# Kernel optimization log

Measured on AMD Instinct MI355X. Metric: run time of the kernel, lower is better.

## Reference

```python
import jax, jax.numpy as jnp
import numpy as np

VOCAB, EMBED, HIDDEN, NCLASS = 50000, 256, 256, 5
B, T = 64, 512


def _lstm_cell(x, h, c, W, U, b):
    # Keras LSTMCell: gate order i, f, g(candidate), o
    z = x @ W + h @ U + b  # [B, 4H]
    i, f, g, o = jnp.split(z, 4, axis=-1)
    i = jax.nn.sigmoid(i)
    f = jax.nn.sigmoid(f)
    g = jnp.tanh(g)
    o = jax.nn.sigmoid(o)
    c_new = f * c + i * g
    h_new = o * jnp.tanh(c_new)
    return h_new, c_new


def _run_stacked(xs, W1, U1, b1, W2, U2, b2):
    # xs: [T, B, E] -> outputs of layer 2: [T, B, H]
    Bb = xs.shape[1]
    H = U1.shape[0]
    zero = jnp.zeros((Bb, H), dtype=xs.dtype)
    init = (zero, zero, zero, zero)

    def step(carry, x_t):
        h1, c1, h2, c2 = carry
        h1, c1 = _lstm_cell(x_t, h1, c1, W1, U1, b1)
        h2, c2 = _lstm_cell(h1, h2, c2, W2, U2, b2)
        return (h1, c1, h2, c2), h2

    _, ys = jax.lax.scan(step, init, xs)
    return ys


def setup_inputs() -> dict:
    key = jax.random.key(0)
    ks = jax.random.split(key, 16)
    s = 0.05

    def mk(k, shape):
        return (jax.random.normal(k, shape, dtype=jnp.float32) * s)

    inp = {
        "tokens": jax.random.randint(ks[0], (B, T), 0, VOCAB, dtype=jnp.int64),
        "embed_table": mk(ks[1], (VOCAB, EMBED)),
        # forward direction, layer 1 and 2
        "fw_W1": mk(ks[2], (EMBED, 4 * HIDDEN)),
        "fw_U1": mk(ks[3], (HIDDEN, 4 * HIDDEN)),
        "fw_b1": jnp.zeros((4 * HIDDEN,), jnp.float32),
        "fw_W2": mk(ks[4], (HIDDEN, 4 * HIDDEN)),
        "fw_U2": mk(ks[5], (HIDDEN, 4 * HIDDEN)),
        "fw_b2": jnp.zeros((4 * HIDDEN,), jnp.float32),
        # backward direction, layer 1 and 2
        "bw_W1": mk(ks[6], (EMBED, 4 * HIDDEN)),
        "bw_U1": mk(ks[7], (HIDDEN, 4 * HIDDEN)),
        "bw_b1": jnp.zeros((4 * HIDDEN,), jnp.float32),
        "bw_W2": mk(ks[8], (HIDDEN, 4 * HIDDEN)),
        "bw_U2": mk(ks[9], (HIDDEN, 4 * HIDDEN)),
        "bw_b2": jnp.zeros((4 * HIDDEN,), jnp.float32),
        # output dense (2H -> 5), softmax
        "dense_W": mk(ks[10], (2 * HIDDEN, NCLASS)),
        "dense_b": jnp.zeros((NCLASS,), jnp.float32),
    }
    return inp


def reference(tokens, embed_table,
              fw_W1, fw_U1, fw_b1, fw_W2, fw_U2, fw_b2,
              bw_W1, bw_U1, bw_b1, bw_W2, bw_U2, bw_b2,
              dense_W, dense_b):
    emb = embed_table[tokens]                    # [B, T, E]
    xs = jnp.swapaxes(emb, 0, 1)                 # [T, B, E]

    ys_fw = _run_stacked(xs, fw_W1, fw_U1, fw_b1, fw_W2, fw_U2, fw_b2)          # [T,B,H]
    ys_bw = _run_stacked(xs[::-1], bw_W1, bw_U1, bw_b1, bw_W2, bw_U2, bw_b2)[::-1]

    feat = jnp.concatenate([ys_fw, ys_bw], axis=-1)   # [T, B, 2H]
    feat = jnp.swapaxes(feat, 0, 1)                   # [B, T, 2H]
    logits = feat @ dense_W + dense_b                 # [B, T, 5]
    return jax.nn.softmax(logits, axis=-1)
```

## Files before the change

### kernel.cpp

```cpp
#include <hip/hip_runtime.h>

typedef __bf16 bf16;
typedef __bf16 bf16x8 __attribute__((ext_vector_type(8)));
typedef float f32x4 __attribute__((ext_vector_type(4)));
typedef unsigned long long u64;

#define T_LEN 512
#define BATCH 64
#define HID 256
#define LDA 520
#define ZLD 68

#define CTRL_BYTES 4096
#define H1_OFF CTRL_BYTES
#define HSLOT_U64 4096
#define HBUF_BYTES (2 * 3 * HSLOT_U64 * 8)
#define H2_OFF (H1_OFF + HBUF_BYTES)
#define LOG_OFF (H2_OFF + HBUF_BYTES)
#define LOG_BYTES (T_LEN * BATCH * 5 * 4)
#define ZERO_BYTES (LOG_OFF + LOG_BYTES)

#define SMEM_A 66560
#define SMEM_Z 17408
#define SMEM_C 4096
#define SMEM_TAIL 576
#define SMEM_BYTES (SMEM_A + SMEM_Z + SMEM_C + SMEM_TAIL)

__device__ inline uint4 cvt8(const float4* s) {
    float4 a = s[0], b = s[1];
    union { uint4 u; bf16 h[8]; } r;
    r.h[0] = (bf16)a.x; r.h[1] = (bf16)a.y; r.h[2] = (bf16)a.z; r.h[3] = (bf16)a.w;
    r.h[4] = (bf16)b.x; r.h[5] = (bf16)b.y; r.h[6] = (bf16)b.z; r.h[7] = (bf16)b.w;
    return r.u;
}

__global__ void __launch_bounds__(256, 1)
lstm_kernel(const int* __restrict__ tokens,
            const float* __restrict__ embed,
            const float* __restrict__ W1f, const float* __restrict__ U1f, const float* __restrict__ b1f,
            const float* __restrict__ W2f, const float* __restrict__ U2f, const float* __restrict__ b2f,
            const float* __restrict__ W1b, const float* __restrict__ U1b, const float* __restrict__ b1b,
            const float* __restrict__ W2b, const float* __restrict__ U2b, const float* __restrict__ b2b,
            const float* __restrict__ dW,
            char* __restrict__ ws)
{
    extern __shared__ char smem[];
    bf16*  Abuf  = (bf16*)smem;
    float* zLds  = (float*)(smem + SMEM_A);
    float* cLds  = (float*)(smem + SMEM_A + SMEM_Z);
    float* bLds  = (float*)(smem + SMEM_A + SMEM_Z + SMEM_C);
    float* dwLds = bLds + 64;

    const int tid = threadIdx.x;
    const int wg  = blockIdx.x;
    const int dir = wg & 1, layer = (wg >> 1) & 1, sub = wg >> 2;

    const float *Wp, *Up, *bp;
    if (dir == 0) { if (layer == 0) { Wp=W1f; Up=U1f; bp=b1f; } else { Wp=W2f; Up=U2f; bp=b2f; } }
    else          { if (layer == 0) { Wp=W1b; Up=U1b; bp=b1b; } else { Wp=W2b; Up=U2b; bp=b2b; } }

    {
        for (int it = 0; it < 32; ++it) {
            int idx = it * 256 + tid;
            int k = idx >> 4, q4 = idx & 15;
            int g = q4 >> 2, u0 = (q4 & 3) * 4;
            const float* src = (k < 256) ? (Wp + (size_t)k * 1024 + g * 256 + sub * 16 + u0)
                                         : (Up + (size_t)(k - 256) * 1024 + g * 256 + sub * 16 + u0);
            float4 v = *(const float4*)src;
            int c0 = g * 16 + u0;
            Abuf[(c0 + 0) * LDA + k] = (bf16)v.x;
            Abuf[(c0 + 1) * LDA + k] = (bf16)v.y;
            Abuf[(c0 + 2) * LDA + k] = (bf16)v.z;
            Abuf[(c0 + 3) * LDA + k] = (bf16)v.w;
        }
        if (tid < 64) {
            int g = tid >> 4, u = tid & 15;
            bLds[tid] = bp[g * 256 + sub * 16 + u];
        }
        if (tid < 80) {
            int u = tid / 5, c = tid % 5;
            dwLds[tid] = dW[(size_t)(dir * 256 + sub * 16 + u) * 5 + c];
        }
        for (int i = tid; i < 1024; i += 256) cLds[i] = 0.f;
    }
    __syncthreads();

    const int wave = tid >> 6, lane = tid & 63, quad = lane >> 4, ln = lane & 15;
    const int mrow0 = (wave >> 1) * 32, ncol0 = (wave & 1) * 32;
    bf16x8 bfrag[2][16];
#pragma unroll
    for (int nt = 0; nt < 2; ++nt)
#pragma unroll
        for (int kt = 0; kt < 16; ++kt)
            bfrag[nt][kt] = *(const bf16x8*)&Abuf[(ncol0 + nt * 16 + ln) * LDA + kt * 32 + quad * 8];
    __syncthreads();

    u64* h1buf = (u64*)(ws + H1_OFF) + (size_t)dir * 3 * HSLOT_U64;
    u64* h2buf = (u64*)(ws + H2_OFF) + (size_t)dir * 3 * HSLOT_U64;
    u64* hOwn  = (layer == 0) ? h1buf : h2buf;
    float* logits   = (float*)(ws + LOG_OFF);
    unsigned* ctrOwn = (unsigned*)ws + (dir * 2 + layer) * 32;
    unsigned* ctrL1  = (unsigned*)ws + (dir * 2 + 0) * 32;
    unsigned* ctrL2  = (unsigned*)ws + (dir * 2 + 1) * 32;

    const int bA = tid >> 2, qA = tid & 3;

    float4 pf[16];
    int tokB = 0;
    if (layer == 0) {
        const int tt0 = dir ? (T_LEN - 1) : 0;
        int tokA = tokens[bA * T_LEN + tt0];
        const float4* src = (const float4*)(embed + (size_t)tokA * HID + qA * 64);
#pragma unroll
        for (int j = 0; j < 16; ++j) pf[j] = src[j];
        const int tt1 = dir ? (T_LEN - 2) : 1;
        tokB = tokens[bA * T_LEN + tt1];
    }

    for (int s = 0; s < T_LEN; ++s) {
        if (tid == 0) {
            unsigned needOwn = (unsigned)s * 16u;
            while (__hip_atomic_load(ctrOwn, __ATOMIC_RELAXED, __HIP_MEMORY_SCOPE_AGENT) < needOwn) {}
            if (layer == 0 && s >= 3) {
                unsigned needT = (unsigned)(s - 2) * 16u;
                while (__hip_atomic_load(ctrL2, __ATOMIC_RELAXED, __HIP_MEMORY_SCOPE_AGENT) < needT) {}
            }
        }
        __syncthreads();

        u64 hreg[16];
        {
            const u64* hsrc = hOwn + (size_t)(s % 3) * HSLOT_U64;
#pragma unroll
            for (int k = 0; k < 16; ++k)
                hreg[k] = __hip_atomic_load(hsrc + k * 256 + tid, __ATOMIC_RELAXED, __HIP_MEMORY_SCOPE_AGENT);
        }
        if (layer == 0) {
            uint4* dstx = (uint4*)&Abuf[bA * LDA + qA * 64];
#pragma unroll
            for (int j = 0; j < 8; ++j) dstx[j] = cvt8(&pf[2 * j]);
        } else {
            if (tid == 0) {
                unsigned needX = (unsigned)(s + 1) * 16u;
                while (__hip_atomic_load(ctrL1, __ATOMIC_RELAXED, __HIP_MEMORY_SCOPE_AGENT) < needX) {}
            }
            __syncthreads();
            u64 xreg[16];
            const u64* xsrc = h1buf + (size_t)((s + 1) % 3) * HSLOT_U64;
#pragma unroll
            for (int k = 0; k < 16; ++k)
                xreg[k] = __hip_atomic_load(xsrc + k * 256 + tid, __ATOMIC_RELAXED, __HIP_MEMORY_SCOPE_AGENT);
#pragma unroll
            for (int k = 0; k < 16; ++k)
                *(u64*)&Abuf[bA * LDA + k * 16 + qA * 4] = xreg[k];
        }
#pragma unroll
        for (int k = 0; k < 16; ++k)
            *(u64*)&Abuf[bA * LDA + 256 + k * 16 + qA * 4] = hreg[k];
        __syncthreads();

        if (layer == 0) {
            const float4* src = (const float4*)(embed + (size_t)tokB * HID + qA * 64);
#pragma unroll
            for (int j = 0; j < 16; ++j) pf[j] = src[j];
            const int sn2 = (s + 2 < T_LEN) ? s + 2 : T_LEN - 1;
            const int tt2 = dir ? (T_LEN - 1 - sn2) : sn2;
            tokB = tokens[bA * T_LEN + tt2];
        }

        f32x4 acc[2][2];
#pragma unroll
        for (int mi = 0; mi < 2; ++mi)
#pragma unroll
            for (int ni = 0; ni < 2; ++ni) acc[mi][ni] = (f32x4)(0.0f);
#pragma unroll
        for (int kt = 0; kt < 16; ++kt) {
            bf16x8 a0 = *(const bf16x8*)&Abuf[(mrow0 + ln) * LDA + kt * 32 + quad * 8];
            bf16x8 a1 = *(const bf16x8*)&Abuf[(mrow0 + 16 + ln) * LDA + kt * 32 + quad * 8];
            acc[0][0] = __builtin_amdgcn_mfma_f32_16x16x32_bf16(a0, bfrag[0][kt], acc[0][0], 0, 0, 0);
            acc[0][1] = __builtin_amdgcn_mfma_f32_16x16x32_bf16(a0, bfrag[1][kt], acc[0][1], 0, 0, 0);
            acc[1][0] = __builtin_amdgcn_mfma_f32_16x16x32_bf16(a1, bfrag[0][kt], acc[1][0], 0, 0, 0);
            acc[1][1] = __builtin_amdgcn_mfma_f32_16x16x32_bf16(a1, bfrag[1][kt], acc[1][1], 0, 0, 0);
        }
#pragma unroll
        for (int mi = 0; mi < 2; ++mi)
#pragma unroll
            for (int ni = 0; ni < 2; ++ni) {
                int row = mrow0 + mi * 16 + quad * 4;
                int col = ncol0 + ni * 16 + ln;
#pragma unroll
                for (int r = 0; r < 4; ++r)
                    zLds[(row + r) * ZLD + col] = acc[mi][ni][r];
            }
        __syncthreads();

        u64* hdst = hOwn + (size_t)((s + 1) % 3) * HSLOT_U64;
        float hv[4];
        {
            const int b = bA, u0 = qA * 4;
#pragma unroll
            for (int e = 0; e < 4; ++e) {
                int u = u0 + e;
                float zi = zLds[b * ZLD + u]      + bLds[u];
                float zf = zLds[b * ZLD + 16 + u] + bLds[16 + u];
                float zg = zLds[b * ZLD + 32 + u] + bLds[32 + u];
                float zo = zLds[b * ZLD + 48 + u] + bLds[48 + u];
                float ig = 1.f / (1.f + __expf(-zi));
                float fg = 1.f / (1.f + __expf(-zf));
                float gg = 1.f - 2.f / (__expf(2.f * zg) + 1.f);
                float og = 1.f / (1.f + __expf(-zo));
                float cn = fg * cLds[b * 16 + u] + ig * gg;
                cLds[b * 16 + u] = cn;
                hv[e] = og * (1.f - 2.f / (__expf(2.f * cn) + 1.f));
            }
            union { u64 w; bf16 h[4]; } pk;
#pragma unroll
            for (int e = 0; e < 4; ++e) pk.h[e] = (bf16)hv[e];
            __hip_atomic_store(hdst + sub * 256 + tid, pk.w,
                               __ATOMIC_RELAXED, __HIP_MEMORY_SCOPE_AGENT);
        }
        float pr[5];
        if (layer == 1) {
#pragma unroll
            for (int c = 0; c < 5; ++c)
                pr[c] = hv[0] * dwLds[(qA * 4 + 0) * 5 + c] + hv[1] * dwLds[(qA * 4 + 1) * 5 + c]
                      + hv[2] * dwLds[(qA * 4 + 2) * 5 + c] + hv[3] * dwLds[(qA * 4 + 3) * 5 + c];
#pragma unroll
            for (int m = 1; m < 4; m <<= 1)
#pragma unroll
                for (int c = 0; c < 5; ++c) pr[c] += __shfl_xor(pr[c], m);
        }

        asm volatile("s_waitcnt vmcnt(0)" ::: "memory");
        __syncthreads();
        if (tid == 0)
            __hip_atomic_fetch_add(ctrOwn, 1u, __ATOMIC_RELAXED, __HIP_MEMORY_SCOPE_AGENT);

        if (layer == 1 && qA == 0) {
            const int tp = dir ? (T_LEN - 1 - s) : s;
            float* lp = &logits[((size_t)tp * BATCH + bA) * 5];
#pragma unroll
            for (int c = 0; c < 5; ++c) atomicAdd(lp + c, pr[c]);
        }
    }
}

__global__ void __launch_bounds__(256)
softmax_kernel(const char* __restrict__ ws, const float* __restrict__ dB, float* __restrict__ out)
{
    const int gid = blockIdx.x * 256 + threadIdx.x;
    const int b = gid & 63, t = gid >> 6;
    const float* lp = (const float*)(ws + LOG_OFF) + ((size_t)t * BATCH + b) * 5;
    float l[5];
#pragma unroll
    for (int c = 0; c < 5; ++c) l[c] = lp[c] + dB[c];
    float m = l[0];
#pragma unroll
    for (int c = 1; c < 5; ++c) m = fmaxf(m, l[c]);
    float e[5], ssum = 0.f;
#pragma unroll
    for (int c = 0; c < 5; ++c) { e[c] = __expf(l[c] - m); ssum += e[c]; }
    float inv = 1.f / ssum;
    float* o = out + ((size_t)b * T_LEN + t) * 5;
#pragma unroll
    for (int c = 0; c < 5; ++c) o[c] = e[c] * inv;
}

extern "C" void kernel_launch(void* const* d_in, const int* in_sizes, int n_in,
                              void* d_out, int out_size, void* d_ws, size_t ws_size,
                              hipStream_t stream)
{
    const int*   tokens = (const int*)d_in[0];
    const float* embed  = (const float*)d_in[1];
    const float* W1f = (const float*)d_in[2],  *U1f = (const float*)d_in[3],  *b1f = (const float*)d_in[4];
    const float* W2f = (const float*)d_in[5],  *U2f = (const float*)d_in[6],  *b2f = (const float*)d_in[7];
    const float* W1b = (const float*)d_in[8],  *U1b = (const float*)d_in[9],  *b1b = (const float*)d_in[10];
    const float* W2b = (const float*)d_in[11], *U2b = (const float*)d_in[12], *b2b = (const float*)d_in[13];
    const float* dW  = (const float*)d_in[14], *dB  = (const float*)d_in[15];

    hipFuncSetAttribute(reinterpret_cast<const void*>(lstm_kernel),
                        hipFuncAttributeMaxDynamicSharedMemorySize, SMEM_BYTES);
    hipMemsetAsync(d_ws, 0, ZERO_BYTES, stream);
    lstm_kernel<<<dim3(64), dim3(256), SMEM_BYTES, stream>>>(
        tokens, embed, W1f, U1f, b1f, W2f, U2f, b2f,
        W1b, U1b, b1b, W2b, U2b, b2b, dW, (char*)d_ws);
    softmax_kernel<<<dim3(128), dim3(256), 0, stream>>>((const char*)d_ws, dB, (float*)d_out);
}
```

Measured before the change: 3.103 ms.

## Replace counter-based step barriers with poisoned data-slot polling

```diff
diff --git a/kernel.cpp b/kernel.cpp
--- a/kernel.cpp
+++ b/kernel.cpp
@@ -8,20 +8,22 @@
 #define T_LEN 512
 #define BATCH 64
 #define HID 256
-#define LDA 520
+#define LDA 528
 #define ZLD 68
 
+#define POISON 0xAAAAAAAAAAAAAAAAull
+
 #define CTRL_BYTES 4096
+#define HSLOT_U64 4096
+#define NSLOT 8
 #define H1_OFF CTRL_BYTES
-#define HSLOT_U64 4096
-#define HBUF_BYTES (2 * 3 * HSLOT_U64 * 8)
+#define HBUF_BYTES (2 * NSLOT * HSLOT_U64 * 8)
 #define H2_OFF (H1_OFF + HBUF_BYTES)
 #define LOG_OFF (H2_OFF + HBUF_BYTES)
 #define LOG_BYTES (T_LEN * BATCH * 5 * 4)
-#define ZERO_BYTES (LOG_OFF + LOG_BYTES)
-
-#define SMEM_A 66560
-#define SMEM_Z 17408
+
+#define SMEM_A (64 * LDA * 2)
+#define SMEM_Z (64 * ZLD * 4)
 #define SMEM_C 4096
 #define SMEM_TAIL 576
 #define SMEM_BYTES (SMEM_A + SMEM_Z + SMEM_C + SMEM_TAIL)
@@ -32,6 +34,16 @@
     r.h[0] = (bf16)a.x; r.h[1] = (bf16)a.y; r.h[2] = (bf16)a.z; r.h[3] = (bf16)a.w;
     r.h[4] = (bf16)b.x; r.h[5] = (bf16)b.y; r.h[6] = (bf16)b.z; r.h[7] = (bf16)b.w;
     return r.u;
+}
+
+__device__ inline void poll16(const u64* base, int tid, u64* v) {
+#pragma unroll
+    for (int k = 0; k < 16; ++k)
+        v[k] = __hip_atomic_load(base + k * 256 + tid, __ATOMIC_RELAXED, __HIP_MEMORY_SCOPE_AGENT);
+#pragma unroll
+    for (int k = 0; k < 16; ++k)
+        while (v[k] == POISON)
+            v[k] = __hip_atomic_load(base + k * 256 + tid, __ATOMIC_RELAXED, __HIP_MEMORY_SCOPE_AGENT);
 }
 
 __global__ void __launch_bounds__(256, 1)
@@ -95,13 +107,11 @@
             bfrag[nt][kt] = *(const bf16x8*)&Abuf[(ncol0 + nt * 16 + ln) * LDA + kt * 32 + quad * 8];
     __syncthreads();
 
-    u64* h1buf = (u64*)(ws + H1_OFF) + (size_t)dir * 3 * HSLOT_U64;
-    u64* h2buf = (u64*)(ws + H2_OFF) + (size_t)dir * 3 * HSLOT_U64;
+    u64* h1buf = (u64*)(ws + H1_OFF) + (size_t)dir * NSLOT * HSLOT_U64;
+    u64* h2buf = (u64*)(ws + H2_OFF) + (size_t)dir * NSLOT * HSLOT_U64;
     u64* hOwn  = (layer == 0) ? h1buf : h2buf;
-    float* logits   = (float*)(ws + LOG_OFF);
-    unsigned* ctrOwn = (unsigned*)ws + (dir * 2 + layer) * 32;
-    unsigned* ctrL1  = (unsigned*)ws + (dir * 2 + 0) * 32;
-    unsigned* ctrL2  = (unsigned*)ws + (dir * 2 + 1) * 32;
+    float* logits = (float*)(ws + LOG_OFF);
+    unsigned* ctrL2 = (unsigned*)ws + dir * 32;
 
     const int bA = tid >> 2, qA = tid & 3;
 
@@ -118,38 +128,22 @@
     }
 
     for (int s = 0; s < T_LEN; ++s) {
-        if (tid == 0) {
-            unsigned needOwn = (unsigned)s * 16u;
-            while (__hip_atomic_load(ctrOwn, __ATOMIC_RELAXED, __HIP_MEMORY_SCOPE_AGENT) < needOwn) {}
-            if (layer == 0 && s >= 3) {
-                unsigned needT = (unsigned)(s - 2) * 16u;
-                while (__hip_atomic_load(ctrL2, __ATOMIC_RELAXED, __HIP_MEMORY_SCOPE_AGENT) < needT) {}
-            }
-        }
-        __syncthreads();
+        if (layer == 0 && tid == 0 && s >= 6) {
+            unsigned need = (unsigned)(s - 5) * 16u;
+            while (__hip_atomic_load(ctrL2, __ATOMIC_RELAXED, __HIP_MEMORY_SCOPE_AGENT) < need)
+                __builtin_amdgcn_s_sleep(1);
+        }
 
         u64 hreg[16];
-        {
-            const u64* hsrc = hOwn + (size_t)(s % 3) * HSLOT_U64;
-#pragma unroll
-            for (int k = 0; k < 16; ++k)
-                hreg[k] = __hip_atomic_load(hsrc + k * 256 + tid, __ATOMIC_RELAXED, __HIP_MEMORY_SCOPE_AGENT);
-        }
+        poll16(hOwn + (size_t)(s & 7) * HSLOT_U64, tid, hreg);
+
         if (layer == 0) {
             uint4* dstx = (uint4*)&Abuf[bA * LDA + qA * 64];
 #pragma unroll
             for (int j = 0; j < 8; ++j) dstx[j] = cvt8(&pf[2 * j]);
         } else {
-            if (tid == 0) {
-                unsigned needX = (unsigned)(s + 1) * 16u;
-                while (__hip_atomic_load(ctrL1, __ATOMIC_RELAXED, __HIP_MEMORY_SCOPE_AGENT) < needX) {}
-            }
-            __syncthreads();
             u64 xreg[16];
-            const u64* xsrc = h1buf + (size_t)((s + 1) % 3) * HSLOT_U64;
-#pragma unroll
-            for (int k = 0; k < 16; ++k)
-                xreg[k] = __hip_atomic_load(xsrc + k * 256 + tid, __ATOMIC_RELAXED, __HIP_MEMORY_SCOPE_AGENT);
+            poll16(h1buf + (size_t)((s + 1) & 7) * HSLOT_U64, tid, xreg);
 #pragma unroll
             for (int k = 0; k < 16; ++k)
                 *(u64*)&Abuf[bA * LDA + k * 16 + qA * 4] = xreg[k];
@@ -194,7 +188,10 @@
             }
         __syncthreads();
 
-        u64* hdst = hOwn + (size_t)((s + 1) % 3) * HSLOT_U64;
+        asm volatile("s_waitcnt vmcnt(0)" ::: "memory");
+
+        u64* hdst = hOwn + (size_t)((s + 1) & 7) * HSLOT_U64;
+        u64* hclr = hOwn + (size_t)((s + 3) & 7) * HSLOT_U64;
         float hv[4];
         {
             const int b = bA, u0 = qA * 4;
@@ -218,9 +215,11 @@
             for (int e = 0; e < 4; ++e) pk.h[e] = (bf16)hv[e];
             __hip_atomic_store(hdst + sub * 256 + tid, pk.w,
                                __ATOMIC_RELAXED, __HIP_MEMORY_SCOPE_AGENT);
-        }
-        float pr[5];
+            __hip_atomic_store(hclr + sub * 256 + tid, POISON,
+                               __ATOMIC_RELAXED, __HIP_MEMORY_SCOPE_AGENT);
+        }
         if (layer == 1) {
+            float pr[5];
 #pragma unroll
             for (int c = 0; c < 5; ++c)
                 pr[c] = hv[0] * dwLds[(qA * 4 + 0) * 5 + c] + hv[1] * dwLds[(qA * 4 + 1) * 5 + c]
@@ -229,19 +228,17 @@
             for (int m = 1; m < 4; m <<= 1)
 #pragma unroll
                 for (int c = 0; c < 5; ++c) pr[c] += __shfl_xor(pr[c], m);
-        }
-
-        asm volatile("s_waitcnt vmcnt(0)" ::: "memory");
+            if (qA == 0) {
+                const int tp = dir ? (T_LEN - 1 - s) : s;
+                float* lp = &logits[((size_t)tp * BATCH + bA) * 5];
+#pragma unroll
+                for (int c = 0; c < 5; ++c) atomicAdd(lp + c, pr[c]);
+            }
+        }
+
         __syncthreads();
-        if (tid == 0)
-            __hip_atomic_fetch_add(ctrOwn, 1u, __ATOMIC_RELAXED, __HIP_MEMORY_SCOPE_AGENT);
-
-        if (layer == 1 && qA == 0) {
-            const int tp = dir ? (T_LEN - 1 - s) : s;
-            float* lp = &logits[((size_t)tp * BATCH + bA) * 5];
-#pragma unroll
-            for (int c = 0; c < 5; ++c) atomicAdd(lp + c, pr[c]);
-        }
+        if (layer == 1 && tid == 0)
+            __hip_atomic_fetch_add(ctrL2, 1u, __ATOMIC_RELAXED, __HIP_MEMORY_SCOPE_AGENT);
     }
 }
 
@@ -278,9 +275,18 @@
     const float* W2b = (const float*)d_in[11], *U2b = (const float*)d_in[12], *b2b = (const float*)d_in[13];
     const float* dW  = (const float*)d_in[14], *dB  = (const float*)d_in[15];
 
+    const size_t DIRB = (size_t)NSLOT * HSLOT_U64 * 8;
+    char* w = (char*)d_ws;
+    hipMemsetAsync(w, 0, CTRL_BYTES, stream);
+    hipMemsetAsync(w + H1_OFF, 0xAA, 2 * HBUF_BYTES, stream);
+    hipMemsetAsync(w + H1_OFF + 0 * DIRB, 0, HSLOT_U64 * 8, stream);
+    hipMemsetAsync(w + H1_OFF + 1 * DIRB, 0, HSLOT_U64 * 8, stream);
+    hipMemsetAsync(w + H2_OFF + 0 * DIRB, 0, HSLOT_U64 * 8, stream);
+    hipMemsetAsync(w + H2_OFF + 1 * DIRB, 0, HSLOT_U64 * 8, stream);
+    hipMemsetAsync(w + LOG_OFF, 0, LOG_BYTES, stream);
+
     hipFuncSetAttribute(reinterpret_cast<const void*>(lstm_kernel),
                         hipFuncAttributeMaxDynamicSharedMemorySize, SMEM_BYTES);
-    hipMemsetAsync(d_ws, 0, ZERO_BYTES, stream);
     lstm_kernel<<<dim3(64), dim3(256), SMEM_BYTES, stream>>>(
         tokens, embed, W1f, U1f, b1f, W2f, U2f, b2f,
         W1b, U1b, b1b, W2b, U2b, b2b, dW, (char*)d_ws);
```

New measurement: 3.317 ms. 6.9% more time.
